# Kernel optimization log

Hardware: AMD Instinct MI355X
Metric: run time of the kernel (lower is better)

The kernel has to match this reference:

```python
import jax, jax.numpy as jnp
import numpy as np

N = 65536
R = 9          # num_relations + 1
D_IN = 256
D_HID = 512
D_OUT = 256
N_HIDDEN = 2


def _xavier(key, shape):
    fan_out, fan_in = shape[-2], shape[-1]
    limit = np.sqrt(6.0 / (fan_in + fan_out))
    return jax.random.uniform(key, shape, jnp.float32, -limit, limit)


def setup_inputs() -> dict:
    key = jax.random.key(0)
    ks = jax.random.split(key, 12)
    inp = {
        "x": jax.random.normal(ks[0], (N, D_IN), jnp.float32),
        "edge_attr": jax.random.uniform(ks[1], (N, R), jnp.float32),
    }
    dims = [(D_HID, D_IN)] + [(D_HID, D_HID)] * N_HIDDEN + [(D_OUT, D_HID)]
    for i, (o, ii) in enumerate(dims):
        inp[f"W{i}"] = _xavier(ks[2 + 2 * i], (R, o, ii))
        inp[f"b{i}"] = _xavier(ks[3 + 2 * i], (R, o))
    return inp


def _linear_kg(x, edge_attr, W, b):
    # roi,ni,nr->no : relation-mixed linear per node
    y = jnp.einsum("roi,ni,nr->no", W, x, edge_attr)
    return y + edge_attr @ b


def reference(x, edge_attr, W0, b0, W1, b1, W2, b2, W3, b3):
    y = jax.nn.relu(_linear_kg(x, edge_attr, W0, b0))
    y = jax.nn.relu(_linear_kg(y, edge_attr, W1, b1))
    y = jax.nn.relu(_linear_kg(y, edge_attr, W2, b2))
    y = _linear_kg(y, edge_attr, W3, b3)
    return y
```

## Files before the change

### kernel.cpp

```cpp
#include <hip/hip_runtime.h>
#include <stdint.h>

using f32x4  = __attribute__((ext_vector_type(4))) float;
using bf16x8 = __attribute__((ext_vector_type(8))) __bf16;

#define GLOAD_LDS16(src, dst) __builtin_amdgcn_global_load_lds(                 \
    (const __attribute__((address_space(1))) void*)(src),                      \
    (__attribute__((address_space(3))) void*)(dst), 16, 0, 0)


__global__ void cvt_x_kernel(const float* __restrict__ x, __bf16* __restrict__ out) {
    const int u    = blockIdx.x * 256 + threadIdx.x;
    const int lane = u & 63;
    const int f    = (u >> 6) & 31;
    const int c    = (u >> 11) & 1;
    const int rb   = u >> 12;
    const int row  = rb * 128 + ((f >> 2) << 4) + (lane & 15);
    const int i    = c * 128 + ((f & 3) << 5) + ((lane >> 4) << 3);
    const float4 a = *(const float4*)(x + (size_t)row * 256 + i);
    const float4 b = *(const float4*)(x + (size_t)row * 256 + i + 4);
    bf16x8 pv;
    pv[0] = (__bf16)a.x; pv[1] = (__bf16)a.y; pv[2] = (__bf16)a.z; pv[3] = (__bf16)a.w;
    pv[4] = (__bf16)b.x; pv[5] = (__bf16)b.y; pv[6] = (__bf16)b.z; pv[7] = (__bf16)b.w;
    *(bf16x8*)(out + (size_t)u * 8) = pv;
}

template<int I, int O>
__global__ void prep_w_kernel(const float* __restrict__ W, __bf16* __restrict__ Bt) {
    constexpr int NCH = I >> 7;
    const int u    = blockIdx.x * 256 + threadIdx.x;
    const int r    = blockIdx.y;
    const int nb   = blockIdx.z;
    const int lane = u & 63;
    const int g    = (u >> 6) & 15;
    const int h    = (u >> 10) & 1;
    const int c    = u >> 11;
    const int mi   = g >> 1;
    const int ks   = (h << 1) + (g & 1);
    const int row  = nb * 128 + mi * 16 + (lane & 15);
    const int i    = c * 128 + ks * 32 + ((lane >> 4) << 3);
    const float* src = W + ((size_t)r * O + row) * I + i;
    const float4 a = *(const float4*)src;
    const float4 b = *(const float4*)(src + 4);
    bf16x8 pv;
    pv[0] = (__bf16)a.x; pv[1] = (__bf16)a.y; pv[2] = (__bf16)a.z; pv[3] = (__bf16)a.w;
    pv[4] = (__bf16)b.x; pv[5] = (__bf16)b.y; pv[6] = (__bf16)b.z; pv[7] = (__bf16)b.w;
    *(bf16x8*)(Bt + ((((size_t)nb * 9 + r) * NCH + c) * 2048 + (u & 2047)) * 8) = pv;
}

template<int O>
__global__ void prep_bias_kernel(const float* __restrict__ b, __bf16* __restrict__ BtB) {
    const int u    = blockIdx.x * 256 + threadIdx.x;
    const int nb   = u >> 10;
    const int q    = u & 1023;
    const int lane = q & 63;
    const int f    = q >> 6;
    const int row  = nb * 128 + ((f >> 1) << 4) + (lane & 15);
    const int kb   = ((f & 1) << 5) + ((lane >> 4) << 3);
    bf16x8 pv;
#pragma unroll
    for (int e = 0; e < 8; ++e) {
        const int k = kb + e;
        pv[e] = (k < 9) ? (__bf16)b[(size_t)k * O + row] : (__bf16)0.f;
    }
    *(bf16x8*)(BtB + (size_t)u * 8) = pv;
}

template<int I, int O, bool RELU, bool OUTF32>
__global__ __launch_bounds__(256, 2)
void kg_gemm(const __bf16* __restrict__ A, const float* __restrict__ E,
             const __bf16* __restrict__ Bt, const __bf16* __restrict__ BtB,
             void* __restrict__ Outv) {
    constexpr int NCH = I >> 7;
    constexpr int NBN = O >> 7;
    static_assert((I & 127) == 0 && (O & 127) == 0, "tile divisibility");

    __shared__ __align__(16) char lds[4 * 16384 + 4608];
    float* const ldsE = (float*)(lds + 65536);

    const int tid  = threadIdx.x;
    const int nwg  = gridDim.x;
    const int braw = blockIdx.x;
    const int bid  = (braw & 7) * (nwg >> 3) + (braw >> 3);
    const int rb   = bid / NBN;
    const int nb   = bid % NBN;
    const int bm0  = rb << 7;
    const int bn0  = nb << 7;
    const int lane = tid & 63;
    const int wid  = tid >> 6;
    const int wr   = (wid >> 1) << 6;
    const int wc   = (wid & 1) << 6;
    const int l15  = lane & 15;
    const int lq   = lane >> 4;

    if (tid < 128) {
        const float* e = E + (size_t)(bm0 + tid) * 9;
#pragma unroll
        for (int q = 0; q < 9; ++q) ldsE[q * 128 + tid] = e[q];
    }

    f32x4 acc[4][4];
#pragma unroll
    for (int m = 0; m < 4; ++m)
#pragma unroll
        for (int n = 0; n < 4; ++n)
            acc[m][n] = f32x4{0.f, 0.f, 0.f, 0.f};
    const f32x4 zero4 = {0.f, 0.f, 0.f, 0.f};

    const size_t Abase = (size_t)rb * NCH * 2048;
    const size_t Bbase = (size_t)nb * 9 * NCH * 2048;
    const int afb = (wr >> 4) << 2;
    const int nfb = (wc >> 4) << 1;

    auto stageS = [&](int s, int c) {
        const __bf16* src = Bt + (Bbase + ((size_t)(s >> 1) * NCH + c) * 2048
                                  + (size_t)((s & 1) << 10)) * 8;
        char* dst = lds + ((s & 3) << 14);
#pragma unroll
        for (int it = 0; it < 4; ++it) {
            const int q = it * 256 + tid;
            GLOAD_LDS16(src + (size_t)q * 8, dst + q * 16);
        }
    };

#pragma unroll 1
    for (int c = 0; c < NCH; ++c) {
        asm volatile("s_waitcnt lgkmcnt(0)" ::: "memory");
        __builtin_amdgcn_s_barrier();
        __builtin_amdgcn_sched_barrier(0);
        bf16x8 af[4][4];
        {
            const __bf16* Ab = A + (Abase + (size_t)c * 2048) * 8;
#pragma unroll
            for (int m = 0; m < 4; ++m)
#pragma unroll
                for (int ks = 0; ks < 4; ++ks)
                    af[m][ks] = *(const bf16x8*)(Ab + ((size_t)((afb + (m << 2) + ks) << 6) + lane) * 8);
        }
        stageS(0, c); stageS(1, c); stageS(2, c); stageS(3, c);
#pragma unroll 1
        for (int r = 0; r < 9; ++r) {
            f32x4 acc2[4][4];
#pragma unroll
            for (int h = 0; h < 2; ++h) {
                const int s = 2 * r + h;
                if (h == 0) {
                    if (r < 8) asm volatile("s_waitcnt vmcnt(12)" ::: "memory");
                    else       asm volatile("s_waitcnt vmcnt(4)"  ::: "memory");
                } else {
                    if (r < 7)      asm volatile("s_waitcnt vmcnt(12)" ::: "memory");
                    else if (r == 7) asm volatile("s_waitcnt vmcnt(8)" ::: "memory");
                    else            asm volatile("s_waitcnt vmcnt(0)"  ::: "memory");
                }
                __builtin_amdgcn_s_barrier();
                __builtin_amdgcn_sched_barrier(0);
                const char* bp = lds + ((s & 3) << 14);
                bf16x8 bv[4][2];
#pragma unroll
                for (int n = 0; n < 4; ++n)
#pragma unroll
                    for (int j = 0; j < 2; ++j)
                        bv[n][j] = *(const bf16x8*)(bp + (((nfb + 2 * n + j) << 6) + lane) * 16);
                asm volatile("s_waitcnt lgkmcnt(0)" ::: "memory");
                __builtin_amdgcn_sched_barrier(0);
                __builtin_amdgcn_s_barrier();
                __builtin_amdgcn_sched_barrier(0);
                if (r < 7) stageS(s + 4, c);
                __builtin_amdgcn_s_setprio(1);
#pragma unroll
                for (int j = 0; j < 2; ++j)
#pragma unroll
                    for (int m = 0; m < 4; ++m)
#pragma unroll
                        for (int n = 0; n < 4; ++n)
                            acc2[m][n] = __builtin_amdgcn_mfma_f32_16x16x32_bf16(
                                af[m][2 * h + j], bv[n][j],
                                (h == 0 && j == 0) ? zero4 : acc2[m][n], 0, 0, 0);
                __builtin_amdgcn_s_setprio(0);
            }
#pragma unroll
            for (int m = 0; m < 4; ++m) {
                const f32x4 ev = *(const f32x4*)(ldsE + r * 128 + wr + m * 16 + lq * 4);
#pragma unroll
                for (int n = 0; n < 4; ++n)
#pragma unroll
                    for (int j = 0; j < 4; ++j)
                        acc[m][n][j] += ev[j] * acc2[m][n][j];
            }
        }
    }

    __syncthreads();
    {
        char* const bufB = lds;
        char* const bufA = lds + 16384;
#pragma unroll
        for (int rr = 0; rr < 4; ++rr) {
            const int q = rr * 256 + tid;
            GLOAD_LDS16(BtB + ((size_t)nb * 1024 + q) * 8, bufB + q * 16);
        }
#pragma unroll
        for (int rr = 0; rr < 4; ++rr) {
            const int q    = rr * 256 + tid;
            const int ln   = q & 63;
            const int f    = q >> 6;
            const int row  = ((f >> 1) << 4) + (ln & 15);
            const int kb   = ((f & 1) << 5) + ((ln >> 4) << 3);
            bf16x8 pv;
#pragma unroll
            for (int e8 = 0; e8 < 8; ++e8) {
                const int k = kb + e8;
                pv[e8] = (k < 9) ? (__bf16)ldsE[k * 128 + row] : (__bf16)0.f;
            }
            *(bf16x8*)(bufA + q * 16) = pv;
        }
        __syncthreads();
#pragma unroll
        for (int ks = 0; ks < 2; ++ks) {
            bf16x8 av[4], bv[4];
#pragma unroll
            for (int m = 0; m < 4; ++m)
                av[m] = *(const bf16x8*)(bufA + (((((wr >> 4) + m) * 2 + ks) << 6) + lane) * 16);
#pragma unroll
            for (int n = 0; n < 4; ++n)
                bv[n] = *(const bf16x8*)(bufB + (((((wc >> 4) + n) * 2 + ks) << 6) + lane) * 16);
#pragma unroll
            for (int m = 0; m < 4; ++m)
#pragma unroll
                for (int n = 0; n < 4; ++n)
                    acc[m][n] = __builtin_amdgcn_mfma_f32_16x16x32_bf16(
                        av[m], bv[n], acc[m][n], 0, 0, 0);
        }
    }

    if (OUTF32) {
        const int orow0 = bm0 + wr + lq * 4;
        const int ocol0 = bn0 + wc + l15;
#pragma unroll
        for (int m = 0; m < 4; ++m)
#pragma unroll
            for (int n = 0; n < 4; ++n)
#pragma unroll
                for (int j = 0; j < 4; ++j) {
                    float v = acc[m][n][j];
                    if (RELU) v = fmaxf(v, 0.f);
                    ((float*)Outv)[(size_t)(orow0 + m * 16 + j) * O + (ocol0 + n * 16)] = v;
                }
    } else {
        constexpr int NCHn = O >> 7;
        __bf16* outp = (__bf16*)Outv;
#pragma unroll
        for (int m = 0; m < 4; ++m) {
#pragma unroll
            for (int n = 0; n < 4; ++n) {
                const int col  = bn0 + wc + n * 16 + l15;
                const int c2   = col >> 7;
                const int f2   = (((wr >> 4) + m) << 2) + ((col >> 5) & 3);
                const int ln2  = ((col >> 3) & 3) * 16 + lq * 4;
                const size_t base =
                    (((size_t)rb * NCHn + c2) * 2048 + f2 * 64 + ln2) * 8 + (col & 7);
#pragma unroll
                for (int j = 0; j < 4; ++j) {
                    float v = acc[m][n][j];
                    if (RELU) v = fmaxf(v, 0.f);
                    outp[base + (size_t)j * 8] = (__bf16)v;
                }
            }
        }
    }
}

extern "C" void kernel_launch(void* const* d_in, const int* in_sizes, int n_in,
                              void* d_out, int out_size, void* d_ws, size_t ws_size,
                              hipStream_t stream) {
    const float* x  = (const float*)d_in[0];
    const float* E  = (const float*)d_in[1];
    const float* W0 = (const float*)d_in[2];
    const float* b0 = (const float*)d_in[3];
    const float* W1 = (const float*)d_in[4];
    const float* b1 = (const float*)d_in[5];
    const float* W2 = (const float*)d_in[6];
    const float* b2 = (const float*)d_in[7];
    const float* W3 = (const float*)d_in[8];
    const float* b3 = (const float*)d_in[9];

    char* ws = (char*)d_ws;
    const size_t actBytes = (size_t)65536 * 512 * 2;
    __bf16* actA = (__bf16*)ws;
    __bf16* actB = (__bf16*)(ws + actBytes);
    char* p = ws + 2 * actBytes;
    __bf16* Bt0 = (__bf16*)p; p += (size_t)4 * 9 * 2 * 2048 * 16;
    __bf16* Bt1 = (__bf16*)p; p += (size_t)4 * 9 * 4 * 2048 * 16;
    __bf16* Bt2 = (__bf16*)p; p += (size_t)4 * 9 * 4 * 2048 * 16;
    __bf16* Bt3 = (__bf16*)p; p += (size_t)2 * 9 * 4 * 2048 * 16;
    __bf16* BtB0 = (__bf16*)p; p += (size_t)4 * 1024 * 16;
    __bf16* BtB1 = (__bf16*)p; p += (size_t)4 * 1024 * 16;
    __bf16* BtB2 = (__bf16*)p; p += (size_t)4 * 1024 * 16;
    __bf16* BtB3 = (__bf16*)p; p += (size_t)2 * 1024 * 16;
    if (ws_size < (size_t)(p - ws)) return;

    cvt_x_kernel<<<dim3(8192), dim3(256), 0, stream>>>(x, actA);
    prep_w_kernel<256, 512><<<dim3(16, 9, 4), dim3(256), 0, stream>>>(W0, Bt0);
    prep_w_kernel<512, 512><<<dim3(32, 9, 4), dim3(256), 0, stream>>>(W1, Bt1);
    prep_w_kernel<512, 512><<<dim3(32, 9, 4), dim3(256), 0, stream>>>(W2, Bt2);
    prep_w_kernel<512, 256><<<dim3(32, 9, 2), dim3(256), 0, stream>>>(W3, Bt3);
    prep_bias_kernel<512><<<dim3(16), dim3(256), 0, stream>>>(b0, BtB0);
    prep_bias_kernel<512><<<dim3(16), dim3(256), 0, stream>>>(b1, BtB1);
    prep_bias_kernel<512><<<dim3(16), dim3(256), 0, stream>>>(b2, BtB2);
    prep_bias_kernel<256><<<dim3(8),  dim3(256), 0, stream>>>(b3, BtB3);

    kg_gemm<256, 512, true,  false><<<dim3(2048), dim3(256), 0, stream>>>(actA, E, Bt0, BtB0, actB);
    kg_gemm<512, 512, true,  false><<<dim3(2048), dim3(256), 0, stream>>>(actB, E, Bt1, BtB1, actA);
    kg_gemm<512, 512, true,  false><<<dim3(2048), dim3(256), 0, stream>>>(actA, E, Bt2, BtB2, actB);
    kg_gemm<512, 256, false, true ><<<dim3(1024), dim3(256), 0, stream>>>(actB, E, Bt3, BtB3, d_out);
}
```

Baseline: 839.8 us.

## Switch GEMM to 32x32x16 MFMA tiles with matching fragment layouts

Replaces the 16x16x32 bf16 MFMA instructions with 32x32x16 ones. The pre-swizzled operand layouts for x, the weights, the bias, the epilogue bias tile and the bf16 inter-layer output all change to match the 32-row fragment shape. Each wave now computes 2x2 tiles of 32x32 instead of 4x4 tiles of 16x16, so it issues fewer MFMA instructions and the A/B fragments get more reuse per instruction. In exchange the layout index math becomes more complex, and per-lane output writes stay scattered as scalar stores.

```diff
diff --git a/kernel.cpp b/kernel.cpp
--- a/kernel.cpp
+++ b/kernel.cpp
@@ -2,6 +2,7 @@
 #include <stdint.h>
 
 using f32x4  = __attribute__((ext_vector_type(4))) float;
+using f32x16 = __attribute__((ext_vector_type(16))) float;
 using bf16x8 = __attribute__((ext_vector_type(8))) __bf16;
 
 #define GLOAD_LDS16(src, dst) __builtin_amdgcn_global_load_lds(                 \
@@ -15,8 +16,8 @@
     const int f    = (u >> 6) & 31;
     const int c    = (u >> 11) & 1;
     const int rb   = u >> 12;
-    const int row  = rb * 128 + ((f >> 2) << 4) + (lane & 15);
-    const int i    = c * 128 + ((f & 3) << 5) + ((lane >> 4) << 3);
+    const int row  = rb * 128 + ((f >> 3) << 5) + (lane & 31);
+    const int i    = c * 128 + ((f & 7) << 4) + ((lane >> 5) << 3);
     const float4 a = *(const float4*)(x + (size_t)row * 256 + i);
     const float4 b = *(const float4*)(x + (size_t)row * 256 + i + 4);
     bf16x8 pv;
@@ -35,11 +36,11 @@
     const int g    = (u >> 6) & 15;
     const int h    = (u >> 10) & 1;
     const int c    = u >> 11;
-    const int mi   = g >> 1;
-    const int ks   = (h << 1) + (g & 1);
-    const int row  = nb * 128 + mi * 16 + (lane & 15);
-    const int i    = c * 128 + ks * 32 + ((lane >> 4) << 3);
-    const float* src = W + ((size_t)r * O + row) * I + i;
+    const int nt   = g >> 2;
+    const int ks16 = (h << 2) + (g & 3);
+    const int o    = nb * 128 + nt * 32 + (lane & 31);
+    const int i    = c * 128 + ks16 * 16 + ((lane >> 5) << 3);
+    const float* src = W + ((size_t)r * O + o) * I + i;
     const float4 a = *(const float4*)src;
     const float4 b = *(const float4*)(src + 4);
     bf16x8 pv;
@@ -55,13 +56,13 @@
     const int q    = u & 1023;
     const int lane = q & 63;
     const int f    = q >> 6;
-    const int row  = nb * 128 + ((f >> 1) << 4) + (lane & 15);
-    const int kb   = ((f & 1) << 5) + ((lane >> 4) << 3);
+    const int o    = nb * 128 + ((f >> 2) << 5) + (lane & 31);
+    const int kb   = ((f & 3) << 4) + ((lane >> 5) << 3);
     bf16x8 pv;
 #pragma unroll
     for (int e = 0; e < 8; ++e) {
         const int k = kb + e;
-        pv[e] = (k < 9) ? (__bf16)b[(size_t)k * O + row] : (__bf16)0.f;
+        pv[e] = (k < 9) ? (__bf16)b[(size_t)k * O + o] : (__bf16)0.f;
     }
     *(bf16x8*)(BtB + (size_t)u * 8) = pv;
 }
@@ -88,10 +89,11 @@
     const int bn0  = nb << 7;
     const int lane = tid & 63;
     const int wid  = tid >> 6;
-    const int wr   = (wid >> 1) << 6;
-    const int wc   = (wid & 1) << 6;
-    const int l15  = lane & 15;
-    const int lq   = lane >> 4;
+    const int mtb  = (wid >> 1) << 1;
+    const int ntb  = (wid & 1) << 1;
+    const int wr64 = mtb << 5;
+    const int l31  = lane & 31;
+    const int lhi  = lane >> 5;
 
     if (tid < 128) {
         const float* e = E + (size_t)(bm0 + tid) * 9;
@@ -99,18 +101,17 @@
         for (int q = 0; q < 9; ++q) ldsE[q * 128 + tid] = e[q];
     }
 
-    f32x4 acc[4][4];
-#pragma unroll
-    for (int m = 0; m < 4; ++m)
-#pragma unroll
-        for (int n = 0; n < 4; ++n)
-            acc[m][n] = f32x4{0.f, 0.f, 0.f, 0.f};
-    const f32x4 zero4 = {0.f, 0.f, 0.f, 0.f};
+    f32x16 zero16;
+#pragma unroll
+    for (int j = 0; j < 16; ++j) zero16[j] = 0.f;
+    f32x16 acc[2][2];
+#pragma unroll
+    for (int mt = 0; mt < 2; ++mt)
+#pragma unroll
+        for (int nt = 0; nt < 2; ++nt) acc[mt][nt] = zero16;
 
     const size_t Abase = (size_t)rb * NCH * 2048;
     const size_t Bbase = (size_t)nb * 9 * NCH * 2048;
-    const int afb = (wr >> 4) << 2;
-    const int nfb = (wc >> 4) << 1;
 
     auto stageS = [&](int s, int c) {
         const __bf16* src = Bt + (Bbase + ((size_t)(s >> 1) * NCH + c) * 2048
@@ -128,19 +129,19 @@
         asm volatile("s_waitcnt lgkmcnt(0)" ::: "memory");
         __builtin_amdgcn_s_barrier();
         __builtin_amdgcn_sched_barrier(0);
-        bf16x8 af[4][4];
+        bf16x8 af[2][8];
         {
             const __bf16* Ab = A + (Abase + (size_t)c * 2048) * 8;
 #pragma unroll
-            for (int m = 0; m < 4; ++m)
-#pragma unroll
-                for (int ks = 0; ks < 4; ++ks)
-                    af[m][ks] = *(const bf16x8*)(Ab + ((size_t)((afb + (m << 2) + ks) << 6) + lane) * 8);
+            for (int mt = 0; mt < 2; ++mt)
+#pragma unroll
+                for (int ks = 0; ks < 8; ++ks)
+                    af[mt][ks] = *(const bf16x8*)(Ab + ((size_t)((((mtb + mt) << 3) + ks) << 6) + lane) * 8);
         }
         stageS(0, c); stageS(1, c); stageS(2, c); stageS(3, c);
 #pragma unroll 1
         for (int r = 0; r < 9; ++r) {
-            f32x4 acc2[4][4];
+            f32x16 acc2[2][2];
 #pragma unroll
             for (int h = 0; h < 2; ++h) {
                 const int s = 2 * r + h;
@@ -148,19 +149,19 @@
                     if (r < 8) asm volatile("s_waitcnt vmcnt(12)" ::: "memory");
                     else       asm volatile("s_waitcnt vmcnt(4)"  ::: "memory");
                 } else {
-                    if (r < 7)      asm volatile("s_waitcnt vmcnt(12)" ::: "memory");
-                    else if (r == 7) asm volatile("s_waitcnt vmcnt(8)" ::: "memory");
-                    else            asm volatile("s_waitcnt vmcnt(0)"  ::: "memory");
+                    if (r < 7)       asm volatile("s_waitcnt vmcnt(12)" ::: "memory");
+                    else if (r == 7) asm volatile("s_waitcnt vmcnt(8)"  ::: "memory");
+                    else             asm volatile("s_waitcnt vmcnt(0)"  ::: "memory");
                 }
                 __builtin_amdgcn_s_barrier();
                 __builtin_amdgcn_sched_barrier(0);
                 const char* bp = lds + ((s & 3) << 14);
-                bf16x8 bv[4][2];
-#pragma unroll
-                for (int n = 0; n < 4; ++n)
-#pragma unroll
-                    for (int j = 0; j < 2; ++j)
-                        bv[n][j] = *(const bf16x8*)(bp + (((nfb + 2 * n + j) << 6) + lane) * 16);
+                bf16x8 bv[2][4];
+#pragma unroll
+                for (int nt = 0; nt < 2; ++nt)
+#pragma unroll
+                    for (int km = 0; km < 4; ++km)
+                        bv[nt][km] = *(const bf16x8*)(bp + (((((ntb + nt) << 2) + km) << 6) + lane) * 16);
                 asm volatile("s_waitcnt lgkmcnt(0)" ::: "memory");
                 __builtin_amdgcn_sched_barrier(0);
                 __builtin_amdgcn_s_barrier();
@@ -168,24 +169,27 @@
                 if (r < 7) stageS(s + 4, c);
                 __builtin_amdgcn_s_setprio(1);
 #pragma unroll
-                for (int j = 0; j < 2; ++j)
-#pragma unroll
-                    for (int m = 0; m < 4; ++m)
-#pragma unroll
-                        for (int n = 0; n < 4; ++n)
-                            acc2[m][n] = __builtin_amdgcn_mfma_f32_16x16x32_bf16(
-                                af[m][2 * h + j], bv[n][j],
-                                (h == 0 && j == 0) ? zero4 : acc2[m][n], 0, 0, 0);
+                for (int km = 0; km < 4; ++km)
+#pragma unroll
+                    for (int mt = 0; mt < 2; ++mt)
+#pragma unroll
+                        for (int nt = 0; nt < 2; ++nt)
+                            acc2[mt][nt] = __builtin_amdgcn_mfma_f32_32x32x16_bf16(
+                                af[mt][(h << 2) + km], bv[nt][km],
+                                (h == 0 && km == 0) ? zero16 : acc2[mt][nt], 0, 0, 0);
                 __builtin_amdgcn_s_setprio(0);
             }
 #pragma unroll
-            for (int m = 0; m < 4; ++m) {
-                const f32x4 ev = *(const f32x4*)(ldsE + r * 128 + wr + m * 16 + lq * 4);
-#pragma unroll
-                for (int n = 0; n < 4; ++n)
-#pragma unroll
-                    for (int j = 0; j < 4; ++j)
-                        acc[m][n][j] += ev[j] * acc2[m][n][j];
+            for (int mt = 0; mt < 2; ++mt) {
+#pragma unroll
+                for (int rq = 0; rq < 4; ++rq) {
+                    const f32x4 ev = *(const f32x4*)(ldsE + r * 128 + wr64 + mt * 32 + rq * 8 + lhi * 4);
+#pragma unroll
+                    for (int nt = 0; nt < 2; ++nt)
+#pragma unroll
+                        for (int jm = 0; jm < 4; ++jm)
+                            acc[mt][nt][rq * 4 + jm] += ev[jm] * acc2[mt][nt][rq * 4 + jm];
+                }
             }
         }
     }
@@ -204,8 +208,8 @@
             const int q    = rr * 256 + tid;
             const int ln   = q & 63;
             const int f    = q >> 6;
-            const int row  = ((f >> 1) << 4) + (ln & 15);
-            const int kb   = ((f & 1) << 5) + ((ln >> 4) << 3);
+            const int row  = ((f >> 2) << 5) + (ln & 31);
+            const int kb   = ((f & 3) << 4) + ((ln >> 5) << 3);
             bf16x8 pv;
 #pragma unroll
             for (int e8 = 0; e8 < 8; ++e8) {
@@ -216,55 +220,62 @@
         }
         __syncthreads();
 #pragma unroll
-        for (int ks = 0; ks < 2; ++ks) {
-            bf16x8 av[4], bv[4];
-#pragma unroll
-            for (int m = 0; m < 4; ++m)
-                av[m] = *(const bf16x8*)(bufA + (((((wr >> 4) + m) * 2 + ks) << 6) + lane) * 16);
-#pragma unroll
-            for (int n = 0; n < 4; ++n)
-                bv[n] = *(const bf16x8*)(bufB + (((((wc >> 4) + n) * 2 + ks) << 6) + lane) * 16);
-#pragma unroll
-            for (int m = 0; m < 4; ++m)
-#pragma unroll
-                for (int n = 0; n < 4; ++n)
-                    acc[m][n] = __builtin_amdgcn_mfma_f32_16x16x32_bf16(
-                        av[m], bv[n], acc[m][n], 0, 0, 0);
+        for (int ks = 0; ks < 4; ++ks) {
+            bf16x8 av[2], bv[2];
+#pragma unroll
+            for (int mt = 0; mt < 2; ++mt)
+                av[mt] = *(const bf16x8*)(bufA + (((((mtb + mt) << 2) + ks) << 6) + lane) * 16);
+#pragma unroll
+            for (int nt = 0; nt < 2; ++nt)
+                bv[nt] = *(const bf16x8*)(bufB + (((((ntb + nt) << 2) + ks) << 6) + lane) * 16);
+#pragma unroll
+            for (int mt = 0; mt < 2; ++mt)
+#pragma unroll
+                for (int nt = 0; nt < 2; ++nt)
+                    acc[mt][nt] = __builtin_amdgcn_mfma_f32_32x32x16_bf16(
+                        av[mt], bv[nt], acc[mt][nt], 0, 0, 0);
         }
     }
 
     if (OUTF32) {
-        const int orow0 = bm0 + wr + lq * 4;
-        const int ocol0 = bn0 + wc + l15;
-#pragma unroll
-        for (int m = 0; m < 4; ++m)
-#pragma unroll
-            for (int n = 0; n < 4; ++n)
-#pragma unroll
-                for (int j = 0; j < 4; ++j) {
-                    float v = acc[m][n][j];
-                    if (RELU) v = fmaxf(v, 0.f);
-                    ((float*)Outv)[(size_t)(orow0 + m * 16 + j) * O + (ocol0 + n * 16)] = v;
-                }
+#pragma unroll
+        for (int mt = 0; mt < 2; ++mt)
+#pragma unroll
+            for (int nt = 0; nt < 2; ++nt) {
+                const int col = bn0 + ((ntb + nt) << 5) + l31;
+#pragma unroll
+                for (int rq = 0; rq < 4; ++rq)
+#pragma unroll
+                    for (int jm = 0; jm < 4; ++jm) {
+                        const int row = bm0 + wr64 + mt * 32 + rq * 8 + lhi * 4 + jm;
+                        float v = acc[mt][nt][rq * 4 + jm];
+                        if (RELU) v = fmaxf(v, 0.f);
+                        ((float*)Outv)[(size_t)row * O + col] = v;
+                    }
+            }
     } else {
         constexpr int NCHn = O >> 7;
         __bf16* outp = (__bf16*)Outv;
 #pragma unroll
-        for (int m = 0; m < 4; ++m) {
-#pragma unroll
-            for (int n = 0; n < 4; ++n) {
-                const int col  = bn0 + wc + n * 16 + l15;
-                const int c2   = col >> 7;
-                const int f2   = (((wr >> 4) + m) << 2) + ((col >> 5) & 3);
-                const int ln2  = ((col >> 3) & 3) * 16 + lq * 4;
-                const size_t base =
-                    (((size_t)rb * NCHn + c2) * 2048 + f2 * 64 + ln2) * 8 + (col & 7);
-#pragma unroll
-                for (int j = 0; j < 4; ++j) {
-                    float v = acc[m][n][j];
-                    if (RELU) v = fmaxf(v, 0.f);
-                    outp[base + (size_t)j * 8] = (__bf16)v;
-                }
+        for (int mt = 0; mt < 2; ++mt) {
+#pragma unroll
+            for (int nt = 0; nt < 2; ++nt) {
+                const int col   = bn0 + ((ntb + nt) << 5) + l31;
+                const int c2    = col >> 7;
+                const int ks2   = (col & 127) >> 4;
+                const int lhi2  = ((l31 >> 3) & 1) << 5;
+                const int e2    = col & 7;
+                const int f2    = ((mtb + mt) << 3) + ks2;
+                const size_t ub = ((size_t)(rb * NCHn + c2) * 2048 + f2 * 64 + lhi2);
+#pragma unroll
+                for (int rq = 0; rq < 4; ++rq)
+#pragma unroll
+                    for (int jm = 0; jm < 4; ++jm) {
+                        const int rlow = rq * 8 + lhi * 4 + jm;
+                        float v = acc[mt][nt][rq * 4 + jm];
+                        if (RELU) v = fmaxf(v, 0.f);
+                        outp[(ub + rlow) * 8 + e2] = (__bf16)v;
+                    }
             }
         }
     }
```

New measurement: 902.4 us. 1.07x slower.

## Double-buffer LDS B-fragment reads and fold edge scaling per half-step

Applied to the files above, without the earlier changes.

Restructures the per-relation inner loop so that B fragments for the next stage are read from LDS into a second register set while MFMAs on the current set run. This removes the second barrier per half-step and the serial LDS read-then-compute dependency. It also drops the 16-tile acc2 accumulator by scaling each two-MFMA partial with the edge weight right away, which cuts register pressure but adds twice as many FMA updates into acc. The vmcnt wait thresholds are re-derived for the new staging order, and getting them wrong could cause stale-data hazards.

```diff
diff --git a/kernel.cpp b/kernel.cpp
--- a/kernel.cpp
+++ b/kernel.cpp
@@ -122,6 +122,14 @@
             GLOAD_LDS16(src + (size_t)q * 8, dst + q * 16);
         }
     };
+    auto readBV = [&](bf16x8 (&bv)[4][2], int s) {
+        const char* bp = lds + ((s & 3) << 14);
+#pragma unroll
+        for (int n = 0; n < 4; ++n)
+#pragma unroll
+            for (int j = 0; j < 2; ++j)
+                bv[n][j] = *(const bf16x8*)(bp + (((nfb + 2 * n + j) << 6) + lane) * 16);
+    };
 
 #pragma unroll 1
     for (int c = 0; c < NCH; ++c) {
@@ -138,54 +146,69 @@
                     af[m][ks] = *(const bf16x8*)(Ab + ((size_t)((afb + (m << 2) + ks) << 6) + lane) * 8);
         }
         stageS(0, c); stageS(1, c); stageS(2, c); stageS(3, c);
+        bf16x8 bvA[4][2], bvB[4][2];
+        asm volatile("s_waitcnt vmcnt(12)" ::: "memory");
+        __builtin_amdgcn_s_barrier();
+        __builtin_amdgcn_sched_barrier(0);
+        readBV(bvA, 0);
+        asm volatile("s_waitcnt lgkmcnt(0)" ::: "memory");
+        __builtin_amdgcn_sched_barrier(0);
+
 #pragma unroll 1
         for (int r = 0; r < 9; ++r) {
-            f32x4 acc2[4][4];
-#pragma unroll
-            for (int h = 0; h < 2; ++h) {
-                const int s = 2 * r + h;
-                if (h == 0) {
-                    if (r < 8) asm volatile("s_waitcnt vmcnt(12)" ::: "memory");
-                    else       asm volatile("s_waitcnt vmcnt(4)"  ::: "memory");
-                } else {
-                    if (r < 7)      asm volatile("s_waitcnt vmcnt(12)" ::: "memory");
-                    else if (r == 7) asm volatile("s_waitcnt vmcnt(8)" ::: "memory");
-                    else            asm volatile("s_waitcnt vmcnt(0)"  ::: "memory");
-                }
+            f32x4 ev[4];
+            {
+                if (r < 8) asm volatile("s_waitcnt vmcnt(8)" ::: "memory");
+                else       asm volatile("s_waitcnt vmcnt(0)" ::: "memory");
                 __builtin_amdgcn_s_barrier();
                 __builtin_amdgcn_sched_barrier(0);
-                const char* bp = lds + ((s & 3) << 14);
-                bf16x8 bv[4][2];
-#pragma unroll
-                for (int n = 0; n < 4; ++n)
-#pragma unroll
-                    for (int j = 0; j < 2; ++j)
-                        bv[n][j] = *(const bf16x8*)(bp + (((nfb + 2 * n + j) << 6) + lane) * 16);
+                readBV(bvB, 2 * r + 1);
+                if (r <= 6) stageS(2 * r + 4, c);
+#pragma unroll
+                for (int m = 0; m < 4; ++m)
+                    ev[m] = *(const f32x4*)(ldsE + r * 128 + wr + m * 16 + lq * 4);
+                __builtin_amdgcn_s_setprio(1);
+#pragma unroll
+                for (int m = 0; m < 4; ++m)
+#pragma unroll
+                    for (int n = 0; n < 4; ++n) {
+                        f32x4 t = __builtin_amdgcn_mfma_f32_16x16x32_bf16(
+                            af[m][0], bvA[n][0], zero4, 0, 0, 0);
+                        t = __builtin_amdgcn_mfma_f32_16x16x32_bf16(
+                            af[m][1], bvA[n][1], t, 0, 0, 0);
+#pragma unroll
+                        for (int j = 0; j < 4; ++j)
+                            acc[m][n][j] += ev[m][j] * t[j];
+                    }
+                __builtin_amdgcn_s_setprio(0);
                 asm volatile("s_waitcnt lgkmcnt(0)" ::: "memory");
                 __builtin_amdgcn_sched_barrier(0);
-                __builtin_amdgcn_s_barrier();
+            }
+            {
+                if (r < 8) {
+                    if (r < 7) asm volatile("s_waitcnt vmcnt(8)" ::: "memory");
+                    else       asm volatile("s_waitcnt vmcnt(4)" ::: "memory");
+                    __builtin_amdgcn_s_barrier();
+                    __builtin_amdgcn_sched_barrier(0);
+                    readBV(bvA, 2 * r + 2);
+                    if (r <= 6) stageS(2 * r + 5, c);
+                }
+                __builtin_amdgcn_s_setprio(1);
+#pragma unroll
+                for (int m = 0; m < 4; ++m)
+#pragma unroll
+                    for (int n = 0; n < 4; ++n) {
+                        f32x4 t = __builtin_amdgcn_mfma_f32_16x16x32_bf16(
+                            af[m][2], bvB[n][0], zero4, 0, 0, 0);
+                        t = __builtin_amdgcn_mfma_f32_16x16x32_bf16(
+                            af[m][3], bvB[n][1], t, 0, 0, 0);
+#pragma unroll
+                        for (int j = 0; j < 4; ++j)
+                            acc[m][n][j] += ev[m][j] * t[j];
+                    }
+                __builtin_amdgcn_s_setprio(0);
+                asm volatile("s_waitcnt lgkmcnt(0)" ::: "memory");
                 __builtin_amdgcn_sched_barrier(0);
-                if (r < 7) stageS(s + 4, c);
-                __builtin_amdgcn_s_setprio(1);
-#pragma unroll
-                for (int j = 0; j < 2; ++j)
-#pragma unroll
-                    for (int m = 0; m < 4; ++m)
-#pragma unroll
-                        for (int n = 0; n < 4; ++n)
-                            acc2[m][n] = __builtin_amdgcn_mfma_f32_16x16x32_bf16(
-                                af[m][2 * h + j], bv[n][j],
-                                (h == 0 && j == 0) ? zero4 : acc2[m][n], 0, 0, 0);
-                __builtin_amdgcn_s_setprio(0);
-            }
-#pragma unroll
-            for (int m = 0; m < 4; ++m) {
-                const f32x4 ev = *(const f32x4*)(ldsE + r * 128 + wr + m * 16 + lq * 4);
-#pragma unroll
-                for (int n = 0; n < 4; ++n)
-#pragma unroll
-                    for (int j = 0; j < 4; ++j)
-                        acc[m][n][j] += ev[j] * acc2[m][n][j];
             }
         }
     }
```

New measurement: 2.063 ms. 146% more time.

## Pre-scale A tiles by relation weights in LDS instead of per-relation accumulator mixing

Applied to the files above, without the earlier changes.

The kernel now multiplies each A chunk by the per-row edge_attr for relation r and writes the bf16 result into LDS. MFMAs then accumulate straight into the final accumulator, which removes the separate acc2 register set and the per-relation FMA epilogue. The A layout is changed to a half-split format so A and B can both be double-buffered in LDS, with the B staging depth cut from four slots to two. In exchange, each relation pass adds a VALU scaling step and LDS writes, and rounds the scaled A to bf16, which changes numerics slightly.

```diff
diff --git a/kernel.cpp b/kernel.cpp
--- a/kernel.cpp
+++ b/kernel.cpp
@@ -12,11 +12,14 @@
 __global__ void cvt_x_kernel(const float* __restrict__ x, __bf16* __restrict__ out) {
     const int u    = blockIdx.x * 256 + threadIdx.x;
     const int lane = u & 63;
-    const int f    = (u >> 6) & 31;
+    const int g    = (u >> 6) & 15;
+    const int h    = (u >> 10) & 1;
     const int c    = (u >> 11) & 1;
     const int rb   = u >> 12;
-    const int row  = rb * 128 + ((f >> 2) << 4) + (lane & 15);
-    const int i    = c * 128 + ((f & 3) << 5) + ((lane >> 4) << 3);
+    const int mi   = g >> 1;
+    const int ks   = (h << 1) + (g & 1);
+    const int row  = rb * 128 + mi * 16 + (lane & 15);
+    const int i    = c * 128 + ks * 32 + ((lane >> 4) << 3);
     const float4 a = *(const float4*)(x + (size_t)row * 256 + i);
     const float4 b = *(const float4*)(x + (size_t)row * 256 + i + 4);
     bf16x8 pv;
@@ -75,7 +78,7 @@
     constexpr int NBN = O >> 7;
     static_assert((I & 127) == 0 && (O & 127) == 0, "tile divisibility");
 
-    __shared__ __align__(16) char lds[4 * 16384 + 4608];
+    __shared__ __align__(16) char lds[65536 + 4608];
     float* const ldsE = (float*)(lds + 65536);
 
     const int tid  = threadIdx.x;
@@ -98,6 +101,8 @@
 #pragma unroll
         for (int q = 0; q < 9; ++q) ldsE[q * 128 + tid] = e[q];
     }
+    asm volatile("s_waitcnt lgkmcnt(0)" ::: "memory");
+    __builtin_amdgcn_s_barrier();
 
     f32x4 acc[4][4];
 #pragma unroll
@@ -105,17 +110,20 @@
 #pragma unroll
         for (int n = 0; n < 4; ++n)
             acc[m][n] = f32x4{0.f, 0.f, 0.f, 0.f};
-    const f32x4 zero4 = {0.f, 0.f, 0.f, 0.f};
-
-    const size_t Abase = (size_t)rb * NCH * 2048;
+
     const size_t Bbase = (size_t)nb * 9 * NCH * 2048;
-    const int afb = (wr >> 4) << 2;
-    const int nfb = (wc >> 4) << 1;
-
-    auto stageS = [&](int s, int c) {
+    const int arow = wr >> 4;
+    const int nfb  = wc >> 4;
+
+    int rowS[4];
+#pragma unroll
+    for (int it = 0; it < 4; ++it)
+        rowS[it] = ((it * 2 + (tid >> 7)) << 4) + (tid & 15);
+
+    auto stageB = [&](int s, int c) {
         const __bf16* src = Bt + (Bbase + ((size_t)(s >> 1) * NCH + c) * 2048
                                   + (size_t)((s & 1) << 10)) * 8;
-        char* dst = lds + ((s & 3) << 14);
+        char* dst = lds + 32768 + ((s & 1) << 14);
 #pragma unroll
         for (int it = 0; it < 4; ++it) {
             const int q = it * 256 + tid;
@@ -123,49 +131,65 @@
         }
     };
 
+    bf16x8 ar[2][4];
+
+    auto scaleA = [&](const bf16x8* arh, int rp, int h) {
+        char* dst = lds + (h << 14);
+#pragma unroll
+        for (int it = 0; it < 4; ++it) {
+            const float ev = ldsE[rp * 128 + rowS[it]];
+            bf16x8 pv;
+#pragma unroll
+            for (int e = 0; e < 8; ++e)
+                pv[e] = (__bf16)((float)arh[it][e] * ev);
+            *(bf16x8*)(dst + (it * 256 + tid) * 16) = pv;
+        }
+    };
+
 #pragma unroll 1
     for (int c = 0; c < NCH; ++c) {
+        const __bf16* Ab = A + (size_t)(rb * NCH + c) * 2048 * 8;
+#pragma unroll
+        for (int h = 0; h < 2; ++h)
+#pragma unroll
+            for (int it = 0; it < 4; ++it)
+                ar[h][it] = *(const bf16x8*)(Ab + ((size_t)((h << 10) + it * 256 + tid)) * 8);
+        stageB(0, c); stageB(1, c);
+        asm volatile("s_waitcnt vmcnt(8)" ::: "memory");
+        scaleA(ar[0], 0, 0);
+        scaleA(ar[1], 0, 1);
         asm volatile("s_waitcnt lgkmcnt(0)" ::: "memory");
-        __builtin_amdgcn_s_barrier();
         __builtin_amdgcn_sched_barrier(0);
-        bf16x8 af[4][4];
-        {
-            const __bf16* Ab = A + (Abase + (size_t)c * 2048) * 8;
-#pragma unroll
-            for (int m = 0; m < 4; ++m)
-#pragma unroll
-                for (int ks = 0; ks < 4; ++ks)
-                    af[m][ks] = *(const bf16x8*)(Ab + ((size_t)((afb + (m << 2) + ks) << 6) + lane) * 8);
-        }
-        stageS(0, c); stageS(1, c); stageS(2, c); stageS(3, c);
+
 #pragma unroll 1
         for (int r = 0; r < 9; ++r) {
-            f32x4 acc2[4][4];
 #pragma unroll
             for (int h = 0; h < 2; ++h) {
-                const int s = 2 * r + h;
-                if (h == 0) {
-                    if (r < 8) asm volatile("s_waitcnt vmcnt(12)" ::: "memory");
-                    else       asm volatile("s_waitcnt vmcnt(4)"  ::: "memory");
-                } else {
-                    if (r < 7)      asm volatile("s_waitcnt vmcnt(12)" ::: "memory");
-                    else if (r == 7) asm volatile("s_waitcnt vmcnt(8)" ::: "memory");
-                    else            asm volatile("s_waitcnt vmcnt(0)"  ::: "memory");
-                }
+                if (r == 8 && h == 1) asm volatile("s_waitcnt vmcnt(0)" ::: "memory");
+                else                  asm volatile("s_waitcnt vmcnt(4)" ::: "memory");
                 __builtin_amdgcn_s_barrier();
                 __builtin_amdgcn_sched_barrier(0);
-                const char* bp = lds + ((s & 3) << 14);
-                bf16x8 bv[4][2];
+                const char* ap = lds + (h << 14);
+                const char* bp = lds + 32768 + (h << 14);
+                bf16x8 av[4][2], bv[4][2];
+#pragma unroll
+                for (int m = 0; m < 4; ++m)
+#pragma unroll
+                    for (int j = 0; j < 2; ++j)
+                        av[m][j] = *(const bf16x8*)(ap + ((((arow + m) * 2 + j) << 6) + lane) * 16);
 #pragma unroll
                 for (int n = 0; n < 4; ++n)
 #pragma unroll
                     for (int j = 0; j < 2; ++j)
-                        bv[n][j] = *(const bf16x8*)(bp + (((nfb + 2 * n + j) << 6) + lane) * 16);
+                        bv[n][j] = *(const bf16x8*)(bp + ((((nfb + n) * 2 + j) << 6) + lane) * 16);
                 asm volatile("s_waitcnt lgkmcnt(0)" ::: "memory");
                 __builtin_amdgcn_sched_barrier(0);
                 __builtin_amdgcn_s_barrier();
                 __builtin_amdgcn_sched_barrier(0);
-                if (r < 7) stageS(s + 4, c);
+                if (r < 8) {
+                    stageB(2 * (r + 1) + h, c);
+                    scaleA(ar[h], r + 1, h);
+                }
                 __builtin_amdgcn_s_setprio(1);
 #pragma unroll
                 for (int j = 0; j < 2; ++j)
@@ -173,19 +197,9 @@
                     for (int m = 0; m < 4; ++m)
 #pragma unroll
                         for (int n = 0; n < 4; ++n)
-                            acc2[m][n] = __builtin_amdgcn_mfma_f32_16x16x32_bf16(
-                                af[m][2 * h + j], bv[n][j],
-                                (h == 0 && j == 0) ? zero4 : acc2[m][n], 0, 0, 0);
+                            acc[m][n] = __builtin_amdgcn_mfma_f32_16x16x32_bf16(
+                                av[m][j], bv[n][j], acc[m][n], 0, 0, 0);
                 __builtin_amdgcn_s_setprio(0);
-            }
-#pragma unroll
-            for (int m = 0; m < 4; ++m) {
-                const f32x4 ev = *(const f32x4*)(ldsE + r * 128 + wr + m * 16 + lq * 4);
-#pragma unroll
-                for (int n = 0; n < 4; ++n)
-#pragma unroll
-                    for (int j = 0; j < 4; ++j)
-                        acc[m][n][j] += ev[j] * acc2[m][n][j];
             }
         }
     }
@@ -255,10 +269,13 @@
             for (int n = 0; n < 4; ++n) {
                 const int col  = bn0 + wc + n * 16 + l15;
                 const int c2   = col >> 7;
-                const int f2   = (((wr >> 4) + m) << 2) + ((col >> 5) & 3);
+                const int ks2  = (col >> 5) & 3;
+                const int mi2  = (wr >> 4) + m;
+                const int g2   = mi2 * 2 + (ks2 & 1);
                 const int ln2  = ((col >> 3) & 3) * 16 + lq * 4;
                 const size_t base =
-                    (((size_t)rb * NCHn + c2) * 2048 + f2 * 64 + ln2) * 8 + (col & 7);
+                    (((size_t)(rb * NCHn + c2) * 2048) + ((size_t)(ks2 >> 1) << 10)
+                     + g2 * 64 + ln2) * 8 + (col & 7);
 #pragma unroll
                 for (int j = 0; j < 4; ++j) {
                     float v = acc[m][n][j];
```

Measured after the change: 1.148 ms. 36.6% more time.
